# Optimization experiments

Measured on AMD Instinct MI355X. Metric: run time of the kernel, lower is better.

The kernel has to match this reference:

```python
import jax, jax.numpy as jnp
import numpy as np

N, S, Q, E, H, D, F, L = 512, 90, 90, 256, 8, 32, 1024, 3  # batch, kv_len, q_len, embed, heads, head_dim, ffn, layers
POS_VOCAB = 90


def setup_inputs() -> dict:
    key = jax.random.key(0)
    ks = jax.random.split(key, 16)
    rn = lambda k, shp, s=0.05: (jax.random.normal(k, shp, jnp.float32) * s)
    return dict(
        x=jax.random.normal(ks[0], (N, S, E), jnp.float32),
        q=jax.random.normal(ks[1], (N, Q, E), jnp.float32),
        positions=jax.random.randint(ks[2], (N, S), 0, POS_VOCAB),
        pos_emb=rn(ks[3], (POS_VOCAB, E), 1.0),
        # per-head-dim Q/K/V projections, SHARED across heads (as in the torch module)
        Wq=rn(ks[4], (L, D, D)), Wk=rn(ks[5], (L, D, D)), Wv=rn(ks[6], (L, D, D)),
        Wo=rn(ks[7], (L, E, E)), bo=jnp.zeros((L, E), jnp.float32),
        g1=jnp.ones((L, E), jnp.float32), b1=jnp.zeros((L, E), jnp.float32),
        g2=jnp.ones((L, E), jnp.float32), b2=jnp.zeros((L, E), jnp.float32),
        Wf1=rn(ks[8], (L, E, F)), bf1=jnp.zeros((L, F), jnp.float32),
        Wf2=rn(ks[9], (L, F, E)), bf2=jnp.zeros((L, E), jnp.float32),
        Wc1=rn(ks[10], (E, 8), 0.1), bc1=jnp.zeros((8,), jnp.float32),
        Wc2=rn(ks[11], (8, 8), 0.1), bc2=jnp.zeros((8,), jnp.float32),
        Wc3=rn(ks[12], (8, 2), 0.1), bc3=jnp.zeros((2,), jnp.float32),
    )


def _ln(x, g, b, eps=1e-5):
    m = jnp.mean(x, -1, keepdims=True)
    v = jnp.mean((x - m) ** 2, -1, keepdims=True)
    return (x - m) * jax.lax.rsqrt(v + eps) * g + b


def _attn(v_in, k_in, q_in, Wv, Wk, Wq, Wo, bo):
    n, kl, _ = k_in.shape
    ql = q_in.shape[1]
    v = jnp.einsum('nkhd,de->nkhe', v_in.reshape(n, kl, H, D), Wv)
    k = jnp.einsum('nkhd,de->nkhe', k_in.reshape(n, kl, H, D), Wk)
    qh = jnp.einsum('nqhd,de->nqhe', q_in.reshape(n, ql, H, D), Wq)
    # note: scale is 1/sqrt(embed_size) as in the original, not 1/sqrt(head_dim)
    att = jax.nn.softmax(jnp.einsum('nqhd,nkhd->nhqk', qh, k) / jnp.sqrt(jnp.float32(E)), axis=-1)
    o = jnp.einsum('nhqk,nkhd->nqhd', att, v).reshape(n, ql, E)
    return o @ Wo + bo


def reference(x, q, positions, pos_emb, Wq, Wk, Wv, Wo, bo, g1, b1, g2, b2,
              Wf1, bf1, Wf2, bf2, Wc1, bc1, Wc2, bc2, Wc3, bc3):
    out = x + pos_emb[positions]           # dropout = identity at eval
    for i in range(L):
        a = _attn(out, out, q, Wv[i], Wk[i], Wq[i], Wo[i], bo[i])
        h = _ln(a + q, g1[i], b1[i])       # residual uses the ORIGINAL q every layer
        f = jax.nn.relu(h @ Wf1[i] + bf1[i]) @ Wf2[i] + bf2[i]
        out = _ln(f + h, g2[i], b2[i])
    z = jnp.tanh(out @ Wc1 + bc1)
    z = jnp.tanh(z @ Wc2 + bc2)
    return jax.nn.sigmoid(z @ Wc3 + bc3)   # [N, Q, 2]
```

## Files before the change

kernel.cpp:

```cpp
#include <hip/hip_runtime.h>

typedef __bf16 bf16x8 __attribute__((ext_vector_type(8)));
typedef __bf16 bf16x4 __attribute__((ext_vector_type(4)));
typedef float f32x4 __attribute__((ext_vector_type(4)));
typedef unsigned short u16x8 __attribute__((ext_vector_type(8)));
typedef unsigned short u16x4 __attribute__((ext_vector_type(4)));

__device__ __forceinline__ unsigned short f2b(float f) {
    union { float f; unsigned int u; } v; v.f = f;
    unsigned int r = v.u + 0x7fffu + ((v.u >> 16) & 1u);
    return (unsigned short)(r >> 16);
}
__device__ __forceinline__ float b2f(unsigned short b) {
    union { unsigned int u; float f; } v; v.u = ((unsigned int)b) << 16;
    return v.f;
}

__device__ __forceinline__ void gll16(const unsigned short* g, unsigned short* l) {
    __builtin_amdgcn_global_load_lds(
        (const __attribute__((address_space(1))) unsigned int*)g,
        (__attribute__((address_space(3))) unsigned int*)l, 16, 0, 0);
}

__global__ __launch_bounds__(256) void prep_wfrag(
    const float* __restrict__ W, unsigned short* __restrict__ dst, int K, int NN)
{
    int k0 = blockIdx.x * 32, n0 = blockIdx.y * 16;
    int KS = K >> 5;
    size_t fbase = ((size_t)(n0 >> 4) * KS + (k0 >> 5)) * 512;
    for (int p = threadIdx.x; p < 512; p += 256) {
        int e = p & 7, lane = p >> 3;
        int n = lane & 15, k = ((lane >> 4) << 3) + e;
        dst[fbase + p] = f2b(W[(size_t)(k0 + k) * NN + n0 + n]);
    }
}

__global__ __launch_bounds__(256) void prep_wT(
    const float* __restrict__ Wq, const float* __restrict__ Wk, const float* __restrict__ Wv,
    unsigned short* __restrict__ wT)
{
    int l = blockIdx.x / 3, w = blockIdx.x % 3;
    const float* src = (w == 0 ? Wq : w == 1 ? Wk : Wv) + (size_t)l * 1024;
    unsigned short* dst = wT + ((size_t)l * 3 + w) * 1024;
    float scale = (w == 0) ? 0.0625f : 1.0f;
    int t = threadIdx.x;
    f32x4 v = *(const f32x4*)&src[t * 4];
    int d = (t * 4) >> 5, j0 = (t * 4) & 31;
    #pragma unroll
    for (int e = 0; e < 4; e++)
        dst[(j0 + e) * 32 + d] = f2b(v[e] * scale);
}

__global__ __launch_bounds__(256) void add_posemb_q(
    const float* __restrict__ x, const int* __restrict__ pos,
    const float* __restrict__ pe, const float* __restrict__ q,
    unsigned short* __restrict__ cur, unsigned short* __restrict__ qb)
{
    size_t row = blockIdx.x;
    int t = threadIdx.x;
    int p = pos[row];
    cur[row * 256 + t] = f2b(x[row * 256 + t] + pe[(size_t)p * 256 + t]);
    qb[row * 256 + t] = f2b(q[row * 256 + t]);
}

__global__ __launch_bounds__(384, 2) void attn_kernel(
    const unsigned short* __restrict__ cur, const unsigned short* __restrict__ qb,
    const unsigned short* __restrict__ wT,
    unsigned short* __restrict__ og)
{
    __shared__ __align__(16) unsigned short qs[96 * 40];
    __shared__ __align__(16) unsigned short ks[96 * 40];
    __shared__ __align__(16) unsigned short vs[96 * 32];

    int nh = blockIdx.x;
    int n = nh >> 3, h = nh & 7;
    int tid = threadIdx.x;
    int wave = tid >> 6, lane = tid & 63;
    int lr = lane & 15, lg = lane >> 4;
    int hiw = lane & 1;

    bf16x8 wq[2], wk[2], wv[2];
    #pragma unroll
    for (int ct = 0; ct < 2; ct++) {
        int o = (ct * 16 + lr) * 32 + lg * 8;
        wq[ct] = *(const bf16x8*)&wT[o];
        wk[ct] = *(const bf16x8*)&wT[1024 + o];
        wv[ct] = *(const bf16x8*)&wT[2048 + o];
    }

    {
        int tile = wave;
        int row = tile * 16 + lr;
        bf16x8 aq = {0,0,0,0,0,0,0,0}, ac = {0,0,0,0,0,0,0,0};
        if (row < 90) {
            size_t base = ((size_t)(n * 90 + row)) * 256 + h * 32 + lg * 8;
            aq = *(const bf16x8*)&qb[base];
            ac = *(const bf16x8*)&cur[base];
        }
        f32x4 zz = {0.f, 0.f, 0.f, 0.f};
        #pragma unroll
        for (int ct = 0; ct < 2; ct++) {
            f32x4 qc = __builtin_amdgcn_mfma_f32_16x16x32_bf16(aq, wq[ct], zz, 0, 0, 0);
            f32x4 kc = __builtin_amdgcn_mfma_f32_16x16x32_bf16(ac, wk[ct], zz, 0, 0, 0);
            f32x4 vc = __builtin_amdgcn_mfma_f32_16x16x32_bf16(ac, wv[ct], zz, 0, 0, 0);
            #pragma unroll
            for (int rr = 0; rr < 4; rr++) {
                float oq = __shfl_xor(qc[rr], 1);
                unsigned a16 = f2b(qc[rr]), o16 = f2b(oq);
                unsigned pk = hiw ? (o16 | (a16 << 16)) : (a16 | (o16 << 16));
                if ((rr >> 1) == hiw)
                    *(unsigned*)&qs[(tile * 16 + lg * 4 + rr) * 40 + ct * 16 + (lr & ~1)] = pk;

                float ok = __shfl_xor(kc[rr], 1);
                a16 = f2b(kc[rr]); o16 = f2b(ok);
                pk = hiw ? (o16 | (a16 << 16)) : (a16 | (o16 << 16));
                if ((rr >> 1) == hiw)
                    *(unsigned*)&ks[(tile * 16 + lg * 4 + rr) * 40 + ct * 16 + (lr & ~1)] = pk;

                float ov = __shfl_xor(vc[rr], 1);
                a16 = f2b(vc[rr]); o16 = f2b(ov);
                pk = hiw ? (o16 | (a16 << 16)) : (a16 | (o16 << 16));
                if ((rr >> 1) == hiw)
                    *(unsigned*)&vs[(tile * 4 + lg) * 128 + ct * 64 + rr * 16 + (lr & ~1)] = pk;
            }
        }
    }
    __syncthreads();

    f32x4 cs[6];
    {
        bf16x8 aq = *(const bf16x8*)&qs[(wave * 16 + lr) * 40 + lg * 8];
        #pragma unroll
        for (int j = 0; j < 6; j++) {
            bf16x8 bk = *(const bf16x8*)&ks[(j * 16 + lr) * 40 + lg * 8];
            f32x4 z = {0.f, 0.f, 0.f, 0.f};
            cs[j] = __builtin_amdgcn_mfma_f32_16x16x32_bf16(bk, aq, z, 0, 0, 0);
        }
    }
    #pragma unroll
    for (int rr = 0; rr < 4; rr++)
        if (lg * 4 + rr >= 10) cs[5][rr] = -1e30f;

    float mx = cs[0][0];
    #pragma unroll
    for (int j = 0; j < 6; j++)
        #pragma unroll
        for (int rr = 0; rr < 4; rr++) mx = fmaxf(mx, cs[j][rr]);
    mx = fmaxf(mx, __shfl_xor(mx, 16));
    mx = fmaxf(mx, __shfl_xor(mx, 32));
    float sum = 0.f;
    #pragma unroll
    for (int j = 0; j < 6; j++)
        #pragma unroll
        for (int rr = 0; rr < 4; rr++) {
            float e = __expf(cs[j][rr] - mx);
            cs[j][rr] = e;
            sum += e;
        }
    sum += __shfl_xor(sum, 16);
    sum += __shfl_xor(sum, 32);
    float inv = 1.f / sum;

    unsigned pk0[6], pk1[6];
    #pragma unroll
    for (int j = 0; j < 6; j++) {
        pk0[j] = (unsigned)f2b(cs[j][0]) | ((unsigned)f2b(cs[j][1]) << 16);
        pk1[j] = (unsigned)f2b(cs[j][2]) | ((unsigned)f2b(cs[j][3]) << 16);
    }

    {
        unsigned vbase = (unsigned)(size_t)&vs[0];
        int sel = lg >> 1;
        int base_lo = lr + ((lg & 1) * 2) * 16;
        int base_hi = base_lo + 16;
        f32x4 oc0 = {0.f,0.f,0.f,0.f}, oc1 = {0.f,0.f,0.f,0.f};
        #pragma unroll
        for (int s = 0; s < 3; s++) {
            unsigned A0 = __shfl(pk0[2*s],     base_lo);
            unsigned A1 = __shfl(pk1[2*s],     base_lo);
            unsigned B0 = __shfl(pk0[2*s + 1], base_lo);
            unsigned B1 = __shfl(pk1[2*s + 1], base_lo);
            unsigned C0 = __shfl(pk0[2*s],     base_hi);
            unsigned C1 = __shfl(pk1[2*s],     base_hi);
            unsigned D0 = __shfl(pk0[2*s + 1], base_hi);
            unsigned D1 = __shfl(pk1[2*s + 1], base_hi);
            union { unsigned u[4]; bf16x8 v; } apu;
            apu.u[0] = sel ? B0 : A0;
            apu.u[1] = sel ? B1 : A1;
            apu.u[2] = sel ? D0 : C0;
            apu.u[3] = sel ? D1 : C1;

            unsigned ta = vbase + (unsigned)((8 * s + 2 * lg) * 256) + (unsigned)(lr * 8);
            bf16x4 b0a, b0b, b1a, b1b;
            asm volatile(
                "ds_read_b64_tr_b16 %0, %4\n\t"
                "ds_read_b64_tr_b16 %1, %4 offset:256\n\t"
                "ds_read_b64_tr_b16 %2, %4 offset:128\n\t"
                "ds_read_b64_tr_b16 %3, %4 offset:384\n\t"
                "s_waitcnt lgkmcnt(0)"
                : "=&v"(b0a), "=&v"(b0b), "=&v"(b1a), "=&v"(b1b)
                : "v"(ta) : "memory");
            __builtin_amdgcn_sched_barrier(0);
            bf16x8 bv0, bv1;
            #pragma unroll
            for (int e = 0; e < 4; e++) {
                bv0[e] = b0a[e]; bv0[4 + e] = b0b[e];
                bv1[e] = b1a[e]; bv1[4 + e] = b1b[e];
            }
            oc0 = __builtin_amdgcn_mfma_f32_16x16x32_bf16(apu.v, bv0, oc0, 0, 0, 0);
            oc1 = __builtin_amdgcn_mfma_f32_16x16x32_bf16(apu.v, bv1, oc1, 0, 0, 0);
        }
        #pragma unroll
        for (int rr = 0; rr < 4; rr++) {
            float invr = __shfl(inv, lg * 4 + rr);
            int row = wave * 16 + lg * 4 + rr;
            if (row < 90) {
                size_t base = ((size_t)(n * 90 + row)) * 256 + h * 32;
                og[base + lr]      = f2b(oc0[rr] * invr);
                og[base + 16 + lr] = f2b(oc1[rr] * invr);
            }
        }
    }
}

__global__ __launch_bounds__(256, 2) void wo_ffn_fused(
    const unsigned short* __restrict__ A,
    const unsigned short* __restrict__ WoFl, const float* __restrict__ bo,
    const unsigned short* __restrict__ qb, const float* __restrict__ g1, const float* __restrict__ b1,
    const unsigned short* __restrict__ W1F, const float* __restrict__ bf1,
    const unsigned short* __restrict__ W2F, const float* __restrict__ bf2,
    const float* __restrict__ g2, const float* __restrict__ b2,
    unsigned short* __restrict__ C)
{
    __shared__ __align__(16) unsigned short As[8 * 2048];
    __shared__ __align__(16) unsigned short hs[8 * 2048];
    __shared__ float ssum[64 * 4], ssq[64 * 4];

    int bx = blockIdx.x;
    bx = (bx & 7) * 90 + (bx >> 3);
    int ra0 = bx * 64;

    int tid = threadIdx.x;
    int wave = tid >> 6, lane = tid & 63;
    int wc = wave;
    int lr = lane & 15, lg = lane >> 4;
    int rsub = lane >> 2, sp = lane & 3;

    #pragma unroll
    for (int kw = 0; kw < 8; kw++) {
        int r = wave * 16 + rsub;
        int sl = sp ^ ((r >> 1) & 3);
        gll16(&A[(size_t)(ra0 + r) * 256 + kw * 32 + sl * 8], &As[kw * 2048 + wave * 512]);
    }
    asm volatile("s_waitcnt vmcnt(0)" ::: "memory");
    __builtin_amdgcn_s_barrier();
    __builtin_amdgcn_sched_barrier(0);

    {
        f32x4 acc[4][4];
        #pragma unroll
        for (int i = 0; i < 4; i++)
            #pragma unroll
            for (int j = 0; j < 4; j++)
                acc[i][j] = (f32x4){0.f, 0.f, 0.f, 0.f};

        int nt0 = wc * 4;
        bf16x8 xa[4], xb[4];
        #pragma unroll
        for (int j = 0; j < 4; j++)
            xa[j] = *(const bf16x8*)&WoFl[((size_t)(nt0 + j) * 8 + 0) * 512 + lane * 8];
        #pragma unroll
        for (int k2 = 0; k2 < 8; k2 += 2) {
            if (k2 + 1 < 8) {
                #pragma unroll
                for (int j = 0; j < 4; j++)
                    xb[j] = *(const bf16x8*)&WoFl[((size_t)(nt0 + j) * 8 + k2 + 1) * 512 + lane * 8];
            }
            {
                bf16x8 ya[4];
                #pragma unroll
                for (int i = 0; i < 4; i++) {
                    int mm = i * 16 + lr;
                    ya[i] = *(const bf16x8*)&As[k2 * 2048 + mm * 32 + (lg ^ ((mm >> 1) & 3)) * 8];
                }
                #pragma unroll
                for (int i = 0; i < 4; i++)
                    #pragma unroll
                    for (int j = 0; j < 4; j++)
                        acc[i][j] = __builtin_amdgcn_mfma_f32_16x16x32_bf16(xa[j], ya[i], acc[i][j], 0, 0, 0);
            }
            if (k2 + 2 < 8) {
                #pragma unroll
                for (int j = 0; j < 4; j++)
                    xa[j] = *(const bf16x8*)&WoFl[((size_t)(nt0 + j) * 8 + k2 + 2) * 512 + lane * 8];
            }
            {
                bf16x8 ya[4];
                #pragma unroll
                for (int i = 0; i < 4; i++) {
                    int mm = i * 16 + lr;
                    ya[i] = *(const bf16x8*)&As[(k2 + 1) * 2048 + mm * 32 + (lg ^ ((mm >> 1) & 3)) * 8];
                }
                #pragma unroll
                for (int i = 0; i < 4; i++)
                    #pragma unroll
                    for (int j = 0; j < 4; j++)
                        acc[i][j] = __builtin_amdgcn_mfma_f32_16x16x32_bf16(xb[j], ya[i], acc[i][j], 0, 0, 0);
            }
        }

        float s1[4] = {0.f,0.f,0.f,0.f}, sq[4] = {0.f,0.f,0.f,0.f};
        #pragma unroll
        for (int i = 0; i < 4; i++) {
            int row = ra0 + i * 16 + lr;
            #pragma unroll
            for (int j = 0; j < 4; j++) {
                int ncol = wc * 64 + j * 16 + lg * 4;
                f32x4 bv = *(const f32x4*)&bo[ncol];
                u16x4 rv = *(const u16x4*)&qb[(size_t)row * 256 + ncol];
                #pragma unroll
                for (int rr = 0; rr < 4; rr++) {
                    acc[i][j][rr] += bv[rr] + b2f(rv[rr]);
                    s1[i] += acc[i][j][rr];
                    sq[i] += acc[i][j][rr] * acc[i][j][rr];
                }
            }
        }
        #pragma unroll
        for (int i = 0; i < 4; i++) {
            s1[i] += __shfl_xor(s1[i], 16);  s1[i] += __shfl_xor(s1[i], 32);
            sq[i] += __shfl_xor(sq[i], 16);  sq[i] += __shfl_xor(sq[i], 32);
            if (lg == 0) {
                int rb = i * 16 + lr;
                ssum[rb * 4 + wc] = s1[i];
                ssq[rb * 4 + wc]  = sq[i];
            }
        }
        __syncthreads();
        #pragma unroll
        for (int i = 0; i < 4; i++) {
            int rb = i * 16 + lr;
            float ts = 0.f, tq = 0.f;
            #pragma unroll
            for (int w = 0; w < 4; w++) { ts += ssum[rb * 4 + w]; tq += ssq[rb * 4 + w]; }
            float mean = ts * (1.f / 256.f);
            float var = tq * (1.f / 256.f) - mean * mean;
            float inv = rsqrtf(var + 1e-5f);
            #pragma unroll
            for (int j = 0; j < 4; j++) {
                int ncol = wc * 64 + j * 16 + lg * 4;
                f32x4 gv = *(const f32x4*)&g1[ncol];
                f32x4 bv = *(const f32x4*)&b1[ncol];
                int row = i * 16 + lr;
                int win = ncol >> 5, cw = ncol & 31;
                int p = (cw >> 3) ^ ((row >> 1) & 3);
                u16x4 ov;
                #pragma unroll
                for (int rr = 0; rr < 4; rr++)
                    ov[rr] = f2b((acc[i][j][rr] - mean) * inv * gv[rr] + bv[rr]);
                *(u16x4*)&hs[win * 2048 + row * 32 + p * 8 + (cw & 7)] = ov;
            }
        }
    }
    __syncthreads();

    f32x4 acc2[4][4];
    #pragma unroll
    for (int i = 0; i < 4; i++)
        #pragma unroll
        for (int j = 0; j < 4; j++)
            acc2[i][j] = (f32x4){0.f, 0.f, 0.f, 0.f};

    #pragma unroll 1
    for (int fc = 0; fc < 4; fc++) {
        f32x4 acc1[4][4];
        #pragma unroll
        for (int i = 0; i < 4; i++)
            #pragma unroll
            for (int j = 0; j < 4; j++)
                acc1[i][j] = (f32x4){0.f, 0.f, 0.f, 0.f};

        int ntb1 = fc * 16 + wc * 4;
        bf16x8 xa[4], xb[4];
        #pragma unroll
        for (int j = 0; j < 4; j++)
            xa[j] = *(const bf16x8*)&W1F[((size_t)(ntb1 + j) * 8 + 0) * 512 + lane * 8];
        #pragma unroll
        for (int k2 = 0; k2 < 8; k2 += 2) {
            if (k2 + 1 < 8) {
                #pragma unroll
                for (int j = 0; j < 4; j++)
                    xb[j] = *(const bf16x8*)&W1F[((size_t)(ntb1 + j) * 8 + k2 + 1) * 512 + lane * 8];
            }
            {
                bf16x8 ya[4];
                #pragma unroll
                for (int i = 0; i < 4; i++) {
                    int mm = i * 16 + lr;
                    ya[i] = *(const bf16x8*)&hs[k2 * 2048 + mm * 32 + (lg ^ ((mm >> 1) & 3)) * 8];
                }
                #pragma unroll
                for (int i = 0; i < 4; i++)
                    #pragma unroll
                    for (int j = 0; j < 4; j++)
                        acc1[i][j] = __builtin_amdgcn_mfma_f32_16x16x32_bf16(xa[j], ya[i], acc1[i][j], 0, 0, 0);
            }
            if (k2 + 2 < 8) {
                #pragma unroll
                for (int j = 0; j < 4; j++)
                    xa[j] = *(const bf16x8*)&W1F[((size_t)(ntb1 + j) * 8 + k2 + 2) * 512 + lane * 8];
            }
            {
                bf16x8 ya[4];
                #pragma unroll
                for (int i = 0; i < 4; i++) {
                    int mm = i * 16 + lr;
                    ya[i] = *(const bf16x8*)&hs[(k2 + 1) * 2048 + mm * 32 + (lg ^ ((mm >> 1) & 3)) * 8];
                }
                #pragma unroll
                for (int i = 0; i < 4; i++)
                    #pragma unroll
                    for (int j = 0; j < 4; j++)
                        acc1[i][j] = __builtin_amdgcn_mfma_f32_16x16x32_bf16(xb[j], ya[i], acc1[i][j], 0, 0, 0);
            }
        }

        __syncthreads();
        #pragma unroll
        for (int i = 0; i < 4; i++) {
            int row = i * 16 + lr;
            #pragma unroll
            for (int j = 0; j < 4; j++) {
                int ncol = wc * 64 + j * 16 + lg * 4;
                f32x4 bv = *(const f32x4*)&bf1[fc * 256 + ncol];
                int win = ncol >> 5, cw = ncol & 31;
                int p = (cw >> 3) ^ ((row >> 1) & 3);
                u16x4 ov;
                #pragma unroll
                for (int rr = 0; rr < 4; rr++)
                    ov[rr] = f2b(fmaxf(acc1[i][j][rr] + bv[rr], 0.f));
                *(u16x4*)&As[win * 2048 + row * 32 + p * 8 + (cw & 7)] = ov;
            }
        }
        __syncthreads();

        int ntb2 = wc * 4;
        #pragma unroll
        for (int j = 0; j < 4; j++)
            xa[j] = *(const bf16x8*)&W2F[((size_t)(ntb2 + j) * 32 + fc * 8 + 0) * 512 + lane * 8];
        #pragma unroll
        for (int k2 = 0; k2 < 8; k2 += 2) {
            if (k2 + 1 < 8) {
                #pragma unroll
                for (int j = 0; j < 4; j++)
                    xb[j] = *(const bf16x8*)&W2F[((size_t)(ntb2 + j) * 32 + fc * 8 + k2 + 1) * 512 + lane * 8];
            }
            {
                bf16x8 ya[4];
                #pragma unroll
                for (int i = 0; i < 4; i++) {
                    int mm = i * 16 + lr;
                    ya[i] = *(const bf16x8*)&As[k2 * 2048 + mm * 32 + (lg ^ ((mm >> 1) & 3)) * 8];
                }
                #pragma unroll
                for (int i = 0; i < 4; i++)
                    #pragma unroll
                    for (int j = 0; j < 4; j++)
                        acc2[i][j] = __builtin_amdgcn_mfma_f32_16x16x32_bf16(xa[j], ya[i], acc2[i][j], 0, 0, 0);
            }
            if (k2 + 2 < 8) {
                #pragma unroll
                for (int j = 0; j < 4; j++)
                    xa[j] = *(const bf16x8*)&W2F[((size_t)(ntb2 + j) * 32 + fc * 8 + k2 + 2) * 512 + lane * 8];
            }
            {
                bf16x8 ya[4];
                #pragma unroll
                for (int i = 0; i < 4; i++) {
                    int mm = i * 16 + lr;
                    ya[i] = *(const bf16x8*)&As[(k2 + 1) * 2048 + mm * 32 + (lg ^ ((mm >> 1) & 3)) * 8];
                }
                #pragma unroll
                for (int i = 0; i < 4; i++)
                    #pragma unroll
                    for (int j = 0; j < 4; j++)
                        acc2[i][j] = __builtin_amdgcn_mfma_f32_16x16x32_bf16(xb[j], ya[i], acc2[i][j], 0, 0, 0);
            }
        }
    }
    __syncthreads();

    float s1[4] = {0.f,0.f,0.f,0.f}, sq[4] = {0.f,0.f,0.f,0.f};
    #pragma unroll
    for (int i = 0; i < 4; i++) {
        int row = i * 16 + lr;
        #pragma unroll
        for (int j = 0; j < 4; j++) {
            int ncol = wc * 64 + j * 16 + lg * 4;
            f32x4 bv = *(const f32x4*)&bf2[ncol];
            int win = ncol >> 5, cw = ncol & 31;
            int p = (cw >> 3) ^ ((row >> 1) & 3);
            u16x4 rv = *(const u16x4*)&hs[win * 2048 + row * 32 + p * 8 + (cw & 7)];
            #pragma unroll
            for (int rr = 0; rr < 4; rr++) {
                acc2[i][j][rr] += bv[rr] + b2f(rv[rr]);
                s1[i] += acc2[i][j][rr];
                sq[i] += acc2[i][j][rr] * acc2[i][j][rr];
            }
        }
    }
    #pragma unroll
    for (int i = 0; i < 4; i++) {
        s1[i] += __shfl_xor(s1[i], 16);  s1[i] += __shfl_xor(s1[i], 32);
        sq[i] += __shfl_xor(sq[i], 16);  sq[i] += __shfl_xor(sq[i], 32);
        if (lg == 0) {
            int rb = i * 16 + lr;
            ssum[rb * 4 + wc] = s1[i];
            ssq[rb * 4 + wc]  = sq[i];
        }
    }
    __syncthreads();
    #pragma unroll
    for (int i = 0; i < 4; i++) {
        int rb = i * 16 + lr;
        float ts = 0.f, tq = 0.f;
        #pragma unroll
        for (int w = 0; w < 4; w++) { ts += ssum[rb * 4 + w]; tq += ssq[rb * 4 + w]; }
        float mean = ts * (1.f / 256.f);
        float var = tq * (1.f / 256.f) - mean * mean;
        float inv = rsqrtf(var + 1e-5f);
        int row = ra0 + rb;
        #pragma unroll
        for (int j = 0; j < 4; j++) {
            int ncol = wc * 64 + j * 16 + lg * 4;
            f32x4 gv = *(const f32x4*)&g2[ncol];
            f32x4 bv = *(const f32x4*)&b2[ncol];
            u16x4 ov;
            #pragma unroll
            for (int rr = 0; rr < 4; rr++)
                ov[rr] = f2b((acc2[i][j][rr] - mean) * inv * gv[rr] + bv[rr]);
            *(u16x4*)&C[(size_t)row * 256 + ncol] = ov;
        }
    }
}

__global__ __launch_bounds__(256) void classifier(
    const unsigned short* __restrict__ xin,
    const float* __restrict__ Wc1, const float* __restrict__ bc1,
    const float* __restrict__ Wc2, const float* __restrict__ bc2,
    const float* __restrict__ Wc3, const float* __restrict__ bc3,
    float* __restrict__ out)
{
    __shared__ float w1[256][9];
    __shared__ float w2[64], b2s[8], w3[16], b3s[2], b1s[8];
    int t = threadIdx.x;
    #pragma unroll
    for (int i = 0; i < 8; i++) {
        int idx = t + i * 256;
        w1[idx >> 3][idx & 7] = Wc1[idx];
    }
    if (t < 64) w2[t] = Wc2[t];
    if (t < 16) w3[t] = Wc3[t];
    if (t < 8) { b2s[t] = bc2[t]; b1s[t] = bc1[t]; }
    if (t < 2) b3s[t] = bc3[t];
    __syncthreads();
    int g = t >> 3, m = t & 7;
    size_t row = (size_t)blockIdx.x * 32 + g;
    float z[8] = {0.f,0.f,0.f,0.f,0.f,0.f,0.f,0.f};
    const unsigned short* xr = xin + row * 256 + m * 32;
    #pragma unroll
    for (int cidx = 0; cidx < 4; cidx++) {
        u16x8 xv = *(const u16x8*)&xr[cidx * 8];
        #pragma unroll
        for (int e = 0; e < 8; e++) {
            float xf = b2f(xv[e]);
            int ei = m * 32 + cidx * 8 + e;
            #pragma unroll
            for (int j = 0; j < 8; j++) z[j] = fmaf(xf, w1[ei][j], z[j]);
        }
    }
    #pragma unroll
    for (int d = 1; d < 8; d <<= 1)
        #pragma unroll
        for (int j = 0; j < 8; j++) z[j] += __shfl_xor(z[j], d);
    float z1[8], z2[8];
    #pragma unroll
    for (int j = 0; j < 8; j++) z1[j] = tanhf(z[j] + b1s[j]);
    #pragma unroll
    for (int j2 = 0; j2 < 8; j2++) {
        float sacc = b2s[j2];
        #pragma unroll
        for (int j = 0; j < 8; j++) sacc = fmaf(z1[j], w2[j * 8 + j2], sacc);
        z2[j2] = tanhf(sacc);
    }
    if (m < 2) {
        float sacc = b3s[m];
        #pragma unroll
        for (int j = 0; j < 8; j++) sacc = fmaf(z2[j], w3[j * 2 + m], sacc);
        out[row * 2 + m] = 1.f / (1.f + __expf(-sacc));
    }
}

extern "C" void kernel_launch(void* const* d_in, const int* in_sizes, int n_in,
                              void* d_out, int out_size, void* d_ws, size_t ws_size,
                              hipStream_t stream) {
    const float* x        = (const float*)d_in[0];
    const float* q        = (const float*)d_in[1];
    const int*   positions= (const int*)d_in[2];
    const float* pos_emb  = (const float*)d_in[3];
    const float* Wq       = (const float*)d_in[4];
    const float* Wk       = (const float*)d_in[5];
    const float* Wv       = (const float*)d_in[6];
    const float* Wo       = (const float*)d_in[7];
    const float* bo       = (const float*)d_in[8];
    const float* g1       = (const float*)d_in[9];
    const float* b1       = (const float*)d_in[10];
    const float* g2       = (const float*)d_in[11];
    const float* b2       = (const float*)d_in[12];
    const float* Wf1      = (const float*)d_in[13];
    const float* bf1      = (const float*)d_in[14];
    const float* Wf2      = (const float*)d_in[15];
    const float* bf2      = (const float*)d_in[16];
    const float* Wc1      = (const float*)d_in[17];
    const float* bc1      = (const float*)d_in[18];
    const float* Wc2      = (const float*)d_in[19];
    const float* bc2      = (const float*)d_in[20];
    const float* Wc3      = (const float*)d_in[21];
    const float* bc3      = (const float*)d_in[22];
    float* out = (float*)d_out;

    const int R = 512 * 90;
    char* ws = (char*)d_ws;
    size_t off = 0;
    auto alloc = [&](size_t bytes) -> void* {
        void* p = ws + off;
        off += (bytes + 255) & ~(size_t)255;
        return p;
    };
    unsigned short* cur = (unsigned short*)alloc((size_t)R * 256 * 2);
    unsigned short* qb  = (unsigned short*)alloc((size_t)R * 256 * 2);
    unsigned short* qho = (unsigned short*)alloc((size_t)R * 256 * 2);
    unsigned short* WoF = (unsigned short*)alloc((size_t)3 * 256 * 256 * 2);
    unsigned short* W1F = (unsigned short*)alloc((size_t)3 * 1024 * 256 * 2);
    unsigned short* W2F = (unsigned short*)alloc((size_t)3 * 256 * 1024 * 2);
    unsigned short* WTqkv = (unsigned short*)alloc((size_t)3 * 3 * 1024 * 2);

    for (int l = 0; l < 3; l++) {
        prep_wfrag<<<dim3(8, 16),  256, 0, stream>>>(Wo  + (size_t)l*256*256,  WoF + (size_t)l*256*256,  256, 256);
        prep_wfrag<<<dim3(8, 64),  256, 0, stream>>>(Wf1 + (size_t)l*256*1024, W1F + (size_t)l*1024*256, 256, 1024);
        prep_wfrag<<<dim3(32, 16), 256, 0, stream>>>(Wf2 + (size_t)l*1024*256, W2F + (size_t)l*256*1024, 1024, 256);
    }
    prep_wT<<<9, 256, 0, stream>>>(Wq, Wk, Wv, WTqkv);
    add_posemb_q<<<R, 256, 0, stream>>>(x, positions, pos_emb, q, cur, qb);

    for (int l = 0; l < 3; l++) {
        attn_kernel<<<512 * 8, 384, 0, stream>>>(cur, qb, WTqkv + (size_t)l * 3 * 1024, qho);
        wo_ffn_fused<<<dim3(720), 256, 0, stream>>>(
            qho, WoF + (size_t)l*256*256, bo + l*256,
            qb, g1 + l*256, b1 + l*256,
            W1F + (size_t)l*1024*256, bf1 + l*1024,
            W2F + (size_t)l*256*1024, bf2 + l*256,
            g2 + l*256, b2 + l*256, cur);
    }
    classifier<<<R / 32, 256, 0, stream>>>(cur, Wc1, bc1, Wc2, bc2, Wc3, bc3, out);
}
```

Measured before the change: 439.1 us.

## Process all eight heads per attention block with prefetch of next head

The attention kernel now launches one block per batch element instead of one per (batch, head) and loops over the eight heads inside the block. While the current head's scores and softmax are computed, it prefetches the next head's Q and input rows from global memory. This amortises the per-block weight-fragment loads and launch overhead across heads. The cost is that only 512 blocks are available to fill the GPU instead of 4096, plus an extra barrier per head, which may reduce latency hiding.

```diff
diff --git a/kernel.cpp b/kernel.cpp
--- a/kernel.cpp
+++ b/kernel.cpp
@@ -72,8 +72,7 @@
     __shared__ __align__(16) unsigned short ks[96 * 40];
     __shared__ __align__(16) unsigned short vs[96 * 32];
 
-    int nh = blockIdx.x;
-    int n = nh >> 3, h = nh & 7;
+    int n = blockIdx.x;
     int tid = threadIdx.x;
     int wave = tid >> 6, lane = tid & 63;
     int lr = lane & 15, lg = lane >> 4;
@@ -88,138 +87,151 @@
         wv[ct] = *(const bf16x8*)&wT[2048 + o];
     }
 
-    {
-        int tile = wave;
-        int row = tile * 16 + lr;
-        bf16x8 aq = {0,0,0,0,0,0,0,0}, ac = {0,0,0,0,0,0,0,0};
-        if (row < 90) {
-            size_t base = ((size_t)(n * 90 + row)) * 256 + h * 32 + lg * 8;
-            aq = *(const bf16x8*)&qb[base];
-            ac = *(const bf16x8*)&cur[base];
-        }
-        f32x4 zz = {0.f, 0.f, 0.f, 0.f};
-        #pragma unroll
-        for (int ct = 0; ct < 2; ct++) {
-            f32x4 qc = __builtin_amdgcn_mfma_f32_16x16x32_bf16(aq, wq[ct], zz, 0, 0, 0);
-            f32x4 kc = __builtin_amdgcn_mfma_f32_16x16x32_bf16(ac, wk[ct], zz, 0, 0, 0);
-            f32x4 vc = __builtin_amdgcn_mfma_f32_16x16x32_bf16(ac, wv[ct], zz, 0, 0, 0);
+    int prow = wave * 16 + lr;
+    bool rowok = prow < 90;
+    size_t rowbase = ((size_t)(n * 90 + prow)) * 256 + lg * 8;
+
+    bf16x8 aq = {0,0,0,0,0,0,0,0}, ac = {0,0,0,0,0,0,0,0};
+    if (rowok) {
+        aq = *(const bf16x8*)&qb[rowbase];
+        ac = *(const bf16x8*)&cur[rowbase];
+    }
+
+    #pragma unroll 1
+    for (int h = 0; h < 8; h++) {
+        {
+            f32x4 zz = {0.f, 0.f, 0.f, 0.f};
+            #pragma unroll
+            for (int ct = 0; ct < 2; ct++) {
+                f32x4 qc = __builtin_amdgcn_mfma_f32_16x16x32_bf16(aq, wq[ct], zz, 0, 0, 0);
+                f32x4 kc = __builtin_amdgcn_mfma_f32_16x16x32_bf16(ac, wk[ct], zz, 0, 0, 0);
+                f32x4 vc = __builtin_amdgcn_mfma_f32_16x16x32_bf16(ac, wv[ct], zz, 0, 0, 0);
+                #pragma unroll
+                for (int rr = 0; rr < 4; rr++) {
+                    float oq = __shfl_xor(qc[rr], 1);
+                    unsigned a16 = f2b(qc[rr]), o16 = f2b(oq);
+                    unsigned pk = hiw ? (o16 | (a16 << 16)) : (a16 | (o16 << 16));
+                    if ((rr >> 1) == hiw)
+                        *(unsigned*)&qs[(wave * 16 + lg * 4 + rr) * 40 + ct * 16 + (lr & ~1)] = pk;
+
+                    float ok = __shfl_xor(kc[rr], 1);
+                    a16 = f2b(kc[rr]); o16 = f2b(ok);
+                    pk = hiw ? (o16 | (a16 << 16)) : (a16 | (o16 << 16));
+                    if ((rr >> 1) == hiw)
+                        *(unsigned*)&ks[(wave * 16 + lg * 4 + rr) * 40 + ct * 16 + (lr & ~1)] = pk;
+
+                    float ov = __shfl_xor(vc[rr], 1);
+                    a16 = f2b(vc[rr]); o16 = f2b(ov);
+                    pk = hiw ? (o16 | (a16 << 16)) : (a16 | (o16 << 16));
+                    if ((rr >> 1) == hiw)
+                        *(unsigned*)&vs[(wave * 4 + lg) * 128 + ct * 64 + rr * 16 + (lr & ~1)] = pk;
+                }
+            }
+        }
+        __syncthreads();
+
+        bf16x8 aqn = {0,0,0,0,0,0,0,0}, acn = {0,0,0,0,0,0,0,0};
+        if (h < 7 && rowok) {
+            aqn = *(const bf16x8*)&qb[rowbase + (h + 1) * 32];
+            acn = *(const bf16x8*)&cur[rowbase + (h + 1) * 32];
+        }
+
+        f32x4 cs[6];
+        {
+            bf16x8 aqf = *(const bf16x8*)&qs[(wave * 16 + lr) * 40 + lg * 8];
+            #pragma unroll
+            for (int j = 0; j < 6; j++) {
+                bf16x8 bk = *(const bf16x8*)&ks[(j * 16 + lr) * 40 + lg * 8];
+                f32x4 z = {0.f, 0.f, 0.f, 0.f};
+                cs[j] = __builtin_amdgcn_mfma_f32_16x16x32_bf16(bk, aqf, z, 0, 0, 0);
+            }
+        }
+        #pragma unroll
+        for (int rr = 0; rr < 4; rr++)
+            if (lg * 4 + rr >= 10) cs[5][rr] = -1e30f;
+
+        float mx = cs[0][0];
+        #pragma unroll
+        for (int j = 0; j < 6; j++)
+            #pragma unroll
+            for (int rr = 0; rr < 4; rr++) mx = fmaxf(mx, cs[j][rr]);
+        mx = fmaxf(mx, __shfl_xor(mx, 16));
+        mx = fmaxf(mx, __shfl_xor(mx, 32));
+        float sum = 0.f;
+        #pragma unroll
+        for (int j = 0; j < 6; j++)
             #pragma unroll
             for (int rr = 0; rr < 4; rr++) {
-                float oq = __shfl_xor(qc[rr], 1);
-                unsigned a16 = f2b(qc[rr]), o16 = f2b(oq);
-                unsigned pk = hiw ? (o16 | (a16 << 16)) : (a16 | (o16 << 16));
-                if ((rr >> 1) == hiw)
-                    *(unsigned*)&qs[(tile * 16 + lg * 4 + rr) * 40 + ct * 16 + (lr & ~1)] = pk;
-
-                float ok = __shfl_xor(kc[rr], 1);
-                a16 = f2b(kc[rr]); o16 = f2b(ok);
-                pk = hiw ? (o16 | (a16 << 16)) : (a16 | (o16 << 16));
-                if ((rr >> 1) == hiw)
-                    *(unsigned*)&ks[(tile * 16 + lg * 4 + rr) * 40 + ct * 16 + (lr & ~1)] = pk;
-
-                float ov = __shfl_xor(vc[rr], 1);
-                a16 = f2b(vc[rr]); o16 = f2b(ov);
-                pk = hiw ? (o16 | (a16 << 16)) : (a16 | (o16 << 16));
-                if ((rr >> 1) == hiw)
-                    *(unsigned*)&vs[(tile * 4 + lg) * 128 + ct * 64 + rr * 16 + (lr & ~1)] = pk;
-            }
-        }
-    }
-    __syncthreads();
-
-    f32x4 cs[6];
-    {
-        bf16x8 aq = *(const bf16x8*)&qs[(wave * 16 + lr) * 40 + lg * 8];
+                float e = __expf(cs[j][rr] - mx);
+                cs[j][rr] = e;
+                sum += e;
+            }
+        sum += __shfl_xor(sum, 16);
+        sum += __shfl_xor(sum, 32);
+        float inv = 1.f / sum;
+
+        unsigned pk0[6], pk1[6];
         #pragma unroll
         for (int j = 0; j < 6; j++) {
-            bf16x8 bk = *(const bf16x8*)&ks[(j * 16 + lr) * 40 + lg * 8];
-            f32x4 z = {0.f, 0.f, 0.f, 0.f};
-            cs[j] = __builtin_amdgcn_mfma_f32_16x16x32_bf16(bk, aq, z, 0, 0, 0);
-        }
-    }
-    #pragma unroll
-    for (int rr = 0; rr < 4; rr++)
-        if (lg * 4 + rr >= 10) cs[5][rr] = -1e30f;
-
-    float mx = cs[0][0];
-    #pragma unroll
-    for (int j = 0; j < 6; j++)
-        #pragma unroll
-        for (int rr = 0; rr < 4; rr++) mx = fmaxf(mx, cs[j][rr]);
-    mx = fmaxf(mx, __shfl_xor(mx, 16));
-    mx = fmaxf(mx, __shfl_xor(mx, 32));
-    float sum = 0.f;
-    #pragma unroll
-    for (int j = 0; j < 6; j++)
-        #pragma unroll
-        for (int rr = 0; rr < 4; rr++) {
-            float e = __expf(cs[j][rr] - mx);
-            cs[j][rr] = e;
-            sum += e;
-        }
-    sum += __shfl_xor(sum, 16);
-    sum += __shfl_xor(sum, 32);
-    float inv = 1.f / sum;
-
-    unsigned pk0[6], pk1[6];
-    #pragma unroll
-    for (int j = 0; j < 6; j++) {
-        pk0[j] = (unsigned)f2b(cs[j][0]) | ((unsigned)f2b(cs[j][1]) << 16);
-        pk1[j] = (unsigned)f2b(cs[j][2]) | ((unsigned)f2b(cs[j][3]) << 16);
-    }
-
-    {
-        unsigned vbase = (unsigned)(size_t)&vs[0];
-        int sel = lg >> 1;
-        int base_lo = lr + ((lg & 1) * 2) * 16;
-        int base_hi = base_lo + 16;
-        f32x4 oc0 = {0.f,0.f,0.f,0.f}, oc1 = {0.f,0.f,0.f,0.f};
-        #pragma unroll
-        for (int s = 0; s < 3; s++) {
-            unsigned A0 = __shfl(pk0[2*s],     base_lo);
-            unsigned A1 = __shfl(pk1[2*s],     base_lo);
-            unsigned B0 = __shfl(pk0[2*s + 1], base_lo);
-            unsigned B1 = __shfl(pk1[2*s + 1], base_lo);
-            unsigned C0 = __shfl(pk0[2*s],     base_hi);
-            unsigned C1 = __shfl(pk1[2*s],     base_hi);
-            unsigned D0 = __shfl(pk0[2*s + 1], base_hi);
-            unsigned D1 = __shfl(pk1[2*s + 1], base_hi);
-            union { unsigned u[4]; bf16x8 v; } apu;
-            apu.u[0] = sel ? B0 : A0;
-            apu.u[1] = sel ? B1 : A1;
-            apu.u[2] = sel ? D0 : C0;
-            apu.u[3] = sel ? D1 : C1;
-
-            unsigned ta = vbase + (unsigned)((8 * s + 2 * lg) * 256) + (unsigned)(lr * 8);
-            bf16x4 b0a, b0b, b1a, b1b;
-            asm volatile(
-                "ds_read_b64_tr_b16 %0, %4\n\t"
-                "ds_read_b64_tr_b16 %1, %4 offset:256\n\t"
-                "ds_read_b64_tr_b16 %2, %4 offset:128\n\t"
-                "ds_read_b64_tr_b16 %3, %4 offset:384\n\t"
-                "s_waitcnt lgkmcnt(0)"
-                : "=&v"(b0a), "=&v"(b0b), "=&v"(b1a), "=&v"(b1b)
-                : "v"(ta) : "memory");
-            __builtin_amdgcn_sched_barrier(0);
-            bf16x8 bv0, bv1;
-            #pragma unroll
-            for (int e = 0; e < 4; e++) {
-                bv0[e] = b0a[e]; bv0[4 + e] = b0b[e];
-                bv1[e] = b1a[e]; bv1[4 + e] = b1b[e];
-            }
-            oc0 = __builtin_amdgcn_mfma_f32_16x16x32_bf16(apu.v, bv0, oc0, 0, 0, 0);
-            oc1 = __builtin_amdgcn_mfma_f32_16x16x32_bf16(apu.v, bv1, oc1, 0, 0, 0);
-        }
-        #pragma unroll
-        for (int rr = 0; rr < 4; rr++) {
-            float invr = __shfl(inv, lg * 4 + rr);
-            int row = wave * 16 + lg * 4 + rr;
-            if (row < 90) {
-                size_t base = ((size_t)(n * 90 + row)) * 256 + h * 32;
-                og[base + lr]      = f2b(oc0[rr] * invr);
-                og[base + 16 + lr] = f2b(oc1[rr] * invr);
-            }
-        }
+            pk0[j] = (unsigned)f2b(cs[j][0]) | ((unsigned)f2b(cs[j][1]) << 16);
+            pk1[j] = (unsigned)f2b(cs[j][2]) | ((unsigned)f2b(cs[j][3]) << 16);
+        }
+
+        {
+            unsigned vbase = (unsigned)(size_t)&vs[0];
+            int sel = lg >> 1;
+            int base_lo = lr + ((lg & 1) * 2) * 16;
+            int base_hi = base_lo + 16;
+            f32x4 oc0 = {0.f,0.f,0.f,0.f}, oc1 = {0.f,0.f,0.f,0.f};
+            #pragma unroll
+            for (int s = 0; s < 3; s++) {
+                unsigned A0 = __shfl(pk0[2*s],     base_lo);
+                unsigned A1 = __shfl(pk1[2*s],     base_lo);
+                unsigned B0 = __shfl(pk0[2*s + 1], base_lo);
+                unsigned B1 = __shfl(pk1[2*s + 1], base_lo);
+                unsigned C0 = __shfl(pk0[2*s],     base_hi);
+                unsigned C1 = __shfl(pk1[2*s],     base_hi);
+                unsigned D0 = __shfl(pk0[2*s + 1], base_hi);
+                unsigned D1 = __shfl(pk1[2*s + 1], base_hi);
+                union { unsigned u[4]; bf16x8 v; } apu;
+                apu.u[0] = sel ? B0 : A0;
+                apu.u[1] = sel ? B1 : A1;
+                apu.u[2] = sel ? D0 : C0;
+                apu.u[3] = sel ? D1 : C1;
+
+                unsigned ta = vbase + (unsigned)((8 * s + 2 * lg) * 256) + (unsigned)(lr * 8);
+                bf16x4 b0a, b0b, b1a, b1b;
+                asm volatile(
+                    "ds_read_b64_tr_b16 %0, %4\n\t"
+                    "ds_read_b64_tr_b16 %1, %4 offset:256\n\t"
+                    "ds_read_b64_tr_b16 %2, %4 offset:128\n\t"
+                    "ds_read_b64_tr_b16 %3, %4 offset:384\n\t"
+                    "s_waitcnt lgkmcnt(0)"
+                    : "=&v"(b0a), "=&v"(b0b), "=&v"(b1a), "=&v"(b1b)
+                    : "v"(ta) : "memory");
+                __builtin_amdgcn_sched_barrier(0);
+                bf16x8 bv0, bv1;
+                #pragma unroll
+                for (int e = 0; e < 4; e++) {
+                    bv0[e] = b0a[e]; bv0[4 + e] = b0b[e];
+                    bv1[e] = b1a[e]; bv1[4 + e] = b1b[e];
+                }
+                oc0 = __builtin_amdgcn_mfma_f32_16x16x32_bf16(apu.v, bv0, oc0, 0, 0, 0);
+                oc1 = __builtin_amdgcn_mfma_f32_16x16x32_bf16(apu.v, bv1, oc1, 0, 0, 0);
+            }
+            #pragma unroll
+            for (int rr = 0; rr < 4; rr++) {
+                float invr = __shfl(inv, lg * 4 + rr);
+                int row = wave * 16 + lg * 4 + rr;
+                if (row < 90) {
+                    size_t base = ((size_t)(n * 90 + row)) * 256 + h * 32;
+                    og[base + lr]      = f2b(oc0[rr] * invr);
+                    og[base + 16 + lr] = f2b(oc1[rr] * invr);
+                }
+            }
+        }
+        __syncthreads();
+        aq = aqn; ac = acn;
     }
 }
 
@@ -654,7 +666,7 @@
     add_posemb_q<<<R, 256, 0, stream>>>(x, positions, pos_emb, q, cur, qb);
 
     for (int l = 0; l < 3; l++) {
-        attn_kernel<<<512 * 8, 384, 0, stream>>>(cur, qb, WTqkv + (size_t)l * 3 * 1024, qho);
+        attn_kernel<<<512, 384, 0, stream>>>(cur, qb, WTqkv + (size_t)l * 3 * 1024, qho);
         wo_ffn_fused<<<dim3(720), 256, 0, stream>>>(
             qho, WoF + (size_t)l*256*256, bo + l*256,
             qb, g1 + l*256, b1 + l*256,
```

Result: slower. 452.7 us (+3.1%).
